# Kernel tuning notes

Hardware: AMD Instinct MI355X
Metric: run time of the kernel (lower is better)

Reference implementation:

```python
import jax, jax.numpy as jnp
import numpy as np

K = 3  # opt.per_pix_kernel


def setup_inputs() -> dict:
    key = jax.random.key(0)
    k1, k2 = jax.random.split(key)
    N, C, H, W = 8, 64, 256, 256
    feature = jax.random.normal(k1, (N, C, H, W), dtype=jnp.float32)
    attention = jax.random.normal(k2, (N, K * K, H, W), dtype=jnp.float32)
    return {"feature": feature, "attention": attention}


def reference(feature, attention):
    # feature: [N, C, H, W]; attention: [N, K^2, H, W]
    # Fused FAC: out[n,c,h,w] = feat + sum_{i,j} feat_pad[n,c,h+i,w+j] * att[n,i*K+j,h,w]
    # Loop over the K*K taps (small fixed set) instead of materializing the
    # [N,H,W,C,K^2] unfolded tensor that the torch code builds.
    N, C, H, W = feature.shape
    pad = (K - 1) // 2
    fp = jnp.pad(feature, ((0, 0), (0, 0), (pad, pad), (pad, pad)))
    out = feature  # residual: origin + FAC(...)
    for i in range(K):
        for j in range(K):
            tap = jax.lax.slice(fp, (0, 0, i, j), (N, C, i + H, j + W))
            out = out + tap * attention[:, i * K + j][:, None, :, :]
    return out
```

## Files before the change

### kernel.cpp

```cpp
#include <hip/hip_runtime.h>


constexpr int N_ = 8, C_ = 64, H_ = 256, W_ = 256;
constexpr int ROWS = 4;
constexpr int CG = 4;
constexpr int CPG = C_ / CG;
constexpr int HB = H_ / ROWS;
constexpr int NWG = N_ * HB * CG;
constexpr int NXCD = 8;
constexpr int NBUF = 3;
constexpr int SLOTS = 8;
constexpr int BUFF = SLOTS * W_;

using f32x4 = __attribute__((ext_vector_type(4))) float;

__global__ __launch_bounds__(256, 4) void fac_kernel(
    const float* __restrict__ feat, const float* __restrict__ att,
    float* __restrict__ out) {
  __shared__ float smem[NBUF * BUFF + W_];
  constexpr int ZROW = NBUF * BUFF;

  int bid = blockIdx.x;
  int lg = (bid % NXCD) * (NWG / NXCD) + bid / NXCD;
  int cg = lg % CG;
  int hb = (lg / CG) % HB;
  int n  = lg / (CG * HB);

  int tx = threadIdx.x & 63;
  int rt = threadIdx.x >> 6;
  int h0 = hb * ROWS;
  int h  = h0 + rt;
  int w4 = tx << 2;

  const size_t plane = (size_t)H_ * W_;

  smem[ZROW + threadIdx.x] = 0.f;

  const float* attp = att + ((size_t)n * 9 * H_ + h) * (size_t)W_ + w4;
  float4 a[9];
#pragma unroll
  for (int t = 0; t < 9; ++t) a[t] = *(const float4*)(attp + (size_t)t * plane);
#pragma unroll
  for (int t = 0; t < 9; ++t)
    asm volatile("" : "+v"(a[t].x), "+v"(a[t].y), "+v"(a[t].z), "+v"(a[t].w));

  const float* fbase = feat + ((size_t)n * C_ + (size_t)cg * CPG) * plane;
  float* obase = out + ((size_t)n * C_ + (size_t)cg * CPG) * plane
                     + (size_t)h * W_ + w4;

  const int s0 = rt * 2, s1 = s0 + 1;
  const int gr0 = min(max(h0 - 1 + s0, 0), H_ - 1);
  const int gr1 = min(max(h0 - 1 + s1, 0), H_ - 1);
  const float* src0 = fbase + (size_t)gr0 * W_ + w4;
  const float* src1 = fbase + (size_t)gr1 * W_ + w4;

  auto STAGE = [&](int ch, int buf) {
    __builtin_amdgcn_global_load_lds(
        (const __attribute__((address_space(1))) uint32_t*)(src0 + (size_t)ch * plane),
        (__attribute__((address_space(3))) uint32_t*)&smem[buf * BUFF + s0 * W_],
        16, 0, 0);
    __builtin_amdgcn_global_load_lds(
        (const __attribute__((address_space(1))) uint32_t*)(src1 + (size_t)ch * plane),
        (__attribute__((address_space(3))) uint32_t*)&smem[buf * BUFF + s1 * W_],
        16, 0, 0);
  };

  const bool hasUp = (h > 0);
  const bool hasDn = (h < H_ - 1);

  STAGE(0, 0);
  STAGE(1, 1);

#pragma unroll
  for (int c = 0; c < CPG; ++c) {
    if (c == 0)
      asm volatile("s_waitcnt vmcnt(0) lgkmcnt(0)\n\ts_barrier" ::: "memory");
    else if (c == CPG - 1)
      asm volatile("s_waitcnt vmcnt(2)\n\ts_barrier" ::: "memory");
    else
      asm volatile("s_waitcnt vmcnt(3)\n\ts_barrier" ::: "memory");

    if (c + 2 < CPG) STAGE(c + 2, (c + 2) % NBUF);

    const int bb = (c % NBUF) * BUFF;
    const float* rA = &smem[hasUp ? bb + rt * W_ : ZROW] + w4;
    const float* rB = &smem[bb + (rt + 1) * W_] + w4;
    const float* rC = &smem[hasDn ? bb + (rt + 2) * W_ : ZROW] + w4;

    float4 f0 = *(const float4*)rA;
    float4 f1 = *(const float4*)rB;
    float4 f2 = *(const float4*)rC;

    float l0 = __shfl_up(f0.w, 1),  l1 = __shfl_up(f1.w, 1),  l2 = __shfl_up(f2.w, 1);
    float r0 = __shfl_down(f0.x, 1), r1 = __shfl_down(f1.x, 1), r2 = __shfl_down(f2.x, 1);
    if (tx == 0)  { l0 = 0.f; l1 = 0.f; l2 = 0.f; }
    if (tx == 63) { r0 = 0.f; r1 = 0.f; r2 = 0.f; }

    float4 acc = f1;
    acc.x += l0   * a[0].x + f0.x * a[1].x + f0.y * a[2].x;
    acc.y += f0.x * a[0].y + f0.y * a[1].y + f0.z * a[2].y;
    acc.z += f0.y * a[0].z + f0.z * a[1].z + f0.w * a[2].z;
    acc.w += f0.z * a[0].w + f0.w * a[1].w + r0   * a[2].w;

    acc.x += l1   * a[3].x + f1.x * a[4].x + f1.y * a[5].x;
    acc.y += f1.x * a[3].y + f1.y * a[4].y + f1.z * a[5].y;
    acc.z += f1.y * a[3].z + f1.z * a[4].z + f1.w * a[5].z;
    acc.w += f1.z * a[3].w + f1.w * a[4].w + r1   * a[5].w;

    acc.x += l2   * a[6].x + f2.x * a[7].x + f2.y * a[8].x;
    acc.y += f2.x * a[6].y + f2.y * a[7].y + f2.z * a[8].y;
    acc.z += f2.y * a[6].z + f2.z * a[7].z + f2.w * a[8].z;
    acc.w += f2.z * a[6].w + f2.w * a[7].w + r2   * a[8].w;

    f32x4 accv = {acc.x, acc.y, acc.z, acc.w};
    __builtin_nontemporal_store(accv, (f32x4*)(obase + (size_t)c * plane));
  }
}

extern "C" void kernel_launch(void* const* d_in, const int* in_sizes, int n_in,
                              void* d_out, int out_size, void* d_ws, size_t ws_size,
                              hipStream_t stream) {
  const float* feat = (const float*)d_in[0];
  const float* att  = (const float*)d_in[1];
  float* out        = (float*)d_out;
  fac_kernel<<<NWG, 256, 0, stream>>>(feat, att, out);
}
```

Before: 47.97 us.

## Give each wave private halo rows to drop block barriers; halve channel groups

Each wave now stages its own three input rows (above, center, below) into a private LDS region, instead of the block sharing one 6-row tile. That removes every s_barrier from the channel loop and leaves only per-wave vmcnt waits, whose counts are retuned to include the interleaved stores. Channel groups drop from 4 to 2, so each workgroup walks twice as many channels and reloads its attention weights fewer times. In exchange, halo rows are fetched redundantly (three loads per wave per channel instead of two), LDS use grows, and there are fewer workgroups in flight.

```diff
diff --git a/kernel.cpp b/kernel.cpp
--- a/kernel.cpp
+++ b/kernel.cpp
@@ -3,22 +3,22 @@
 
 constexpr int N_ = 8, C_ = 64, H_ = 256, W_ = 256;
 constexpr int ROWS = 4;
-constexpr int CG = 4;
+constexpr int CG = 2;
 constexpr int CPG = C_ / CG;
 constexpr int HB = H_ / ROWS;
 constexpr int NWG = N_ * HB * CG;
 constexpr int NXCD = 8;
 constexpr int NBUF = 3;
-constexpr int SLOTS = 8;
-constexpr int BUFF = SLOTS * W_;
+constexpr int WROWS = 3;
+constexpr int BUFW = ROWS * WROWS * W_;
+constexpr int ZROW = NBUF * BUFW;
 
 using f32x4 = __attribute__((ext_vector_type(4))) float;
 
 __global__ __launch_bounds__(256, 4) void fac_kernel(
     const float* __restrict__ feat, const float* __restrict__ att,
     float* __restrict__ out) {
-  __shared__ float smem[NBUF * BUFF + W_];
-  constexpr int ZROW = NBUF * BUFF;
+  __shared__ float smem[NBUF * BUFW + W_];
 
   int bid = blockIdx.x;
   int lg = (bid % NXCD) * (NWG / NXCD) + bid / NXCD;
@@ -34,7 +34,10 @@
 
   const size_t plane = (size_t)H_ * W_;
 
-  smem[ZROW + threadIdx.x] = 0.f;
+  {
+    f32x4 z = {0.f, 0.f, 0.f, 0.f};
+    *(f32x4*)&smem[ZROW + w4] = z;
+  }
 
   const float* attp = att + ((size_t)n * 9 * H_ + h) * (size_t)W_ + w4;
   float4 a[9];
@@ -48,21 +51,23 @@
   float* obase = out + ((size_t)n * C_ + (size_t)cg * CPG) * plane
                      + (size_t)h * W_ + w4;
 
-  const int s0 = rt * 2, s1 = s0 + 1;
-  const int gr0 = min(max(h0 - 1 + s0, 0), H_ - 1);
-  const int gr1 = min(max(h0 - 1 + s1, 0), H_ - 1);
-  const float* src0 = fbase + (size_t)gr0 * W_ + w4;
-  const float* src1 = fbase + (size_t)gr1 * W_ + w4;
+  const int g0 = max(h - 1, 0), g2 = min(h + 1, H_ - 1);
+  const float* src0 = fbase + (size_t)g0 * W_ + w4;
+  const float* src1 = fbase + (size_t)h  * W_ + w4;
+  const float* src2 = fbase + (size_t)g2 * W_ + w4;
+  const int wb = rt * WROWS * W_;
 
   auto STAGE = [&](int ch, int buf) {
+    const int b = buf * BUFW + wb;
     __builtin_amdgcn_global_load_lds(
         (const __attribute__((address_space(1))) uint32_t*)(src0 + (size_t)ch * plane),
-        (__attribute__((address_space(3))) uint32_t*)&smem[buf * BUFF + s0 * W_],
-        16, 0, 0);
+        (__attribute__((address_space(3))) uint32_t*)&smem[b], 16, 0, 0);
     __builtin_amdgcn_global_load_lds(
         (const __attribute__((address_space(1))) uint32_t*)(src1 + (size_t)ch * plane),
-        (__attribute__((address_space(3))) uint32_t*)&smem[buf * BUFF + s1 * W_],
-        16, 0, 0);
+        (__attribute__((address_space(3))) uint32_t*)&smem[b + W_], 16, 0, 0);
+    __builtin_amdgcn_global_load_lds(
+        (const __attribute__((address_space(1))) uint32_t*)(src2 + (size_t)ch * plane),
+        (__attribute__((address_space(3))) uint32_t*)&smem[b + 2 * W_], 16, 0, 0);
   };
 
   const bool hasUp = (h > 0);
@@ -74,18 +79,20 @@
 #pragma unroll
   for (int c = 0; c < CPG; ++c) {
     if (c == 0)
-      asm volatile("s_waitcnt vmcnt(0) lgkmcnt(0)\n\ts_barrier" ::: "memory");
+      asm volatile("s_waitcnt vmcnt(3)" ::: "memory");
+    else if (c == 1)
+      asm volatile("s_waitcnt vmcnt(4)" ::: "memory");
     else if (c == CPG - 1)
-      asm volatile("s_waitcnt vmcnt(2)\n\ts_barrier" ::: "memory");
+      asm volatile("s_waitcnt vmcnt(2)" ::: "memory");
     else
-      asm volatile("s_waitcnt vmcnt(3)\n\ts_barrier" ::: "memory");
+      asm volatile("s_waitcnt vmcnt(5)" ::: "memory");
 
     if (c + 2 < CPG) STAGE(c + 2, (c + 2) % NBUF);
 
-    const int bb = (c % NBUF) * BUFF;
-    const float* rA = &smem[hasUp ? bb + rt * W_ : ZROW] + w4;
-    const float* rB = &smem[bb + (rt + 1) * W_] + w4;
-    const float* rC = &smem[hasDn ? bb + (rt + 2) * W_ : ZROW] + w4;
+    const int bb = (c % NBUF) * BUFW + wb;
+    const float* rA = hasUp ? &smem[bb] + w4 : &smem[ZROW] + w4;
+    const float* rB = &smem[bb + W_] + w4;
+    const float* rC = hasDn ? &smem[bb + 2 * W_] + w4 : &smem[ZROW] + w4;
 
     float4 f0 = *(const float4*)rA;
     float4 f1 = *(const float4*)rB;
```

Measured after the change: 45.70 us. 4.7% less time.
